# Performance work log

Measured on AMD Instinct MI355X. Metric: run time of the kernel, lower is better.

Reference implementation:

```python
import jax, jax.numpy as jnp
import numpy as np

EPS = 1e-5
SCALE = 30.0

def _ln(x, g, b):
    m = jnp.mean(x, axis=-1, keepdims=True)
    v = jnp.mean((x - m) ** 2, axis=-1, keepdims=True)
    return (x - m) * jax.lax.rsqrt(v + EPS) * g + b

def setup_inputs() -> dict:
    key = jax.random.key(0)
    ks = jax.random.split(key, 12)
    B, L, K, H, NIN = 4, 2048, 48, 128, 512
    s = 0.02
    return {
        "h_V": jax.random.normal(ks[0], (B, L, H), jnp.float32),
        "h_E": jax.random.normal(ks[1], (B, L, K, NIN - H), jnp.float32),
        "mask_V": jnp.ones((B, L), jnp.float32),
        "mask_E": jnp.ones((B, L, K), jnp.float32),
        "w1": jax.random.normal(ks[2], (NIN, H), jnp.float32) * s,
        "b1": jnp.zeros((H,), jnp.float32),
        "w2": jax.random.normal(ks[3], (H, H), jnp.float32) * s,
        "b2": jnp.zeros((H,), jnp.float32),
        "w3": jax.random.normal(ks[4], (H, H), jnp.float32) * s,
        "b3": jnp.zeros((H,), jnp.float32),
        "g1": jnp.ones((H,), jnp.float32),
        "bn1": jnp.zeros((H,), jnp.float32),
        "g2": jnp.ones((H,), jnp.float32),
        "bn2": jnp.zeros((H,), jnp.float32),
        "wf1": jax.random.normal(ks[5], (H, 4 * H), jnp.float32) * s,
        "bf1": jnp.zeros((4 * H,), jnp.float32),
        "wf2": jax.random.normal(ks[6], (4 * H, H), jnp.float32) * s,
        "bf2": jnp.zeros((H,), jnp.float32),
    }

def reference(h_V, h_E, mask_V, mask_E, w1, b1, w2, b2, w3, b3, g1, bn1, g2, bn2, wf1, bf1, wf2, bf2):
    B, L, H = h_V.shape
    K = h_E.shape[-2]
    gelu = lambda x: jax.nn.gelu(x, approximate=False)  # torch nn.GELU default (erf)
    # expand source node over K neighbors and concat: (B,L,K,num_in)
    h_V_exp = jnp.broadcast_to(h_V[:, :, None, :], (B, L, K, H))
    h_EV = jnp.concatenate([h_V_exp, h_E], axis=-1)
    h_msg = gelu(jnp.einsum('blki,ih->blkh', h_EV, w1) + b1)
    h_msg = gelu(jnp.einsum('blkh,hj->blkj', h_msg, w2) + b2)
    h_msg = jnp.einsum('blkh,hj->blkj', h_msg, w3) + b3
    h_msg = mask_E[..., None] * h_msg
    dh = jnp.sum(h_msg, axis=-2) / SCALE  # masked sum-aggregate over K
    h = _ln(h_V + dh, g1, bn1)
    dff = jnp.einsum('blh,hf->blf', h, wf1) + bf1
    dff = jnp.einsum('blf,fh->blh', gelu(dff), wf2) + bf2
    h = _ln(h + dff, g2, bn2)
    return mask_V[..., None] * h
```

## Files before the change

kernel.cpp:

```cpp
#include <hip/hip_runtime.h>
#include <hip/hip_bf16.h>


typedef __bf16 bf16x8 __attribute__((ext_vector_type(8)));
typedef float f32x4 __attribute__((ext_vector_type(4)));

#define HH 128
#define EE 384
#define KK 48

__device__ __forceinline__ float gelu_f(float x) {
  float x2 = x * x;
  float u = x * (-1.5957691216f - 0.0713548163f * x2);
  float e = __expf(u);
  return __fdividef(x, 1.0f + e);
}

__device__ __forceinline__ bf16x8 cvt8(float4 a, float4 b) {
  bf16x8 r;
  r[0] = (__bf16)a.x; r[1] = (__bf16)a.y; r[2] = (__bf16)a.z; r[3] = (__bf16)a.w;
  r[4] = (__bf16)b.x; r[5] = (__bf16)b.y; r[6] = (__bf16)b.z; r[7] = (__bf16)b.w;
  return r;
}

__device__ __forceinline__ f32x4 mfma16(bf16x8 a, bf16x8 b, f32x4 c) {
  return __builtin_amdgcn_mfma_f32_16x16x32_bf16(a, b, c, 0, 0, 0);
}

__global__ void prep_kernel(const float* __restrict__ w1, const float* __restrict__ w2,
                            const float* __restrict__ w3, const float* __restrict__ wf1,
                            const float* __restrict__ wf2, __bf16* __restrict__ out) {
  int idx = blockIdx.x * 256 + threadIdx.x;
  if (idx < 49152) {
    int n = idx / 384, e = idx - n * 384;
    out[idx] = (__bf16)w1[(128 + e) * 128 + n];
  } else if (idx < 65536) {
    int t = idx - 49152; int j = t >> 7, h = t & 127;
    out[idx] = (__bf16)w2[h * 128 + j];
  } else if (idx < 81920) {
    int t = idx - 65536; int j = t >> 7, h = t & 127;
    out[idx] = (__bf16)w3[h * 128 + j];
  } else if (idx < 147456) {
    int t = idx - 81920; int f = t >> 7, h = t & 127;
    out[idx] = (__bf16)wf1[h * 512 + f];
  } else if (idx < 212992) {
    int t = idx - 147456; int h = t >> 9, f = t & 511;
    out[idx] = (__bf16)wf2[f * 128 + h];
  }
}

__global__ __launch_bounds__(128) void v1_kernel(const float* __restrict__ hV,
                                                 const float* __restrict__ w1,
                                                 const float* __restrict__ b1,
                                                 float* __restrict__ V1) {
  __shared__ __align__(16) float sV[16][128];
  const int tid = threadIdx.x;
  const long p0 = (long)blockIdx.x * 16;
  for (int i = 0; i < 16; ++i) sV[i][tid] = hV[(p0 + i) * HH + tid];
  __syncthreads();
  float acc[16];
  float bb = b1[tid];
  #pragma unroll
  for (int p = 0; p < 16; ++p) acc[p] = bb;
  for (int k = 0; k < 128; k += 4) {
    float wa = w1[(k + 0) * HH + tid];
    float wb = w1[(k + 1) * HH + tid];
    float wc = w1[(k + 2) * HH + tid];
    float wd = w1[(k + 3) * HH + tid];
    #pragma unroll
    for (int p = 0; p < 16; ++p) {
      float4 h4 = *(const float4*)&sV[p][k];
      acc[p] = fmaf(h4.x, wa, fmaf(h4.y, wb, fmaf(h4.z, wc, fmaf(h4.w, wd, acc[p]))));
    }
  }
  #pragma unroll
  for (int p = 0; p < 16; ++p) V1[(p0 + p) * HH + tid] = acc[p];
}

__global__ __launch_bounds__(256, 2) void msg_kernel(
    const float* __restrict__ hE, const float* __restrict__ hV,
    const float* __restrict__ maskE,
    const __bf16* __restrict__ w1t, const __bf16* __restrict__ w2t,
    const __bf16* __restrict__ w3t, const float* __restrict__ V1,
    const float* __restrict__ b2, const float* __restrict__ b3,
    const float* __restrict__ g1, const float* __restrict__ bn1,
    float* __restrict__ outH) {
  __shared__ __align__(16) __bf16 sA[192][40];
  __shared__ __align__(16) __bf16 sB[128][40];
  __shared__ __align__(16) __bf16 sH[192][136];
  __shared__ float sDH[4][128];
  __shared__ float sMask[192];

  const int tid = threadIdx.x;
  const int lane = tid & 63;
  const int w = tid >> 6;
  const long pos0 = (long)blockIdx.x * 4;
  const long rowBase = pos0 * KK;
  const int fr = lane & 15;
  const int fg = lane >> 4;

  if (tid < 192) sMask[tid] = maskE[rowBase + tid];

  f32x4 acc[3][8];
  #pragma unroll
  for (int m = 0; m < 3; ++m)
    #pragma unroll
    for (int n = 0; n < 8; ++n) acc[m][n] = (f32x4){0.f, 0.f, 0.f, 0.f};

  const int srow = tid >> 2;
  const int scol = (tid & 3) * 8;

  for (int kc = 0; kc < 12; ++kc) {
    const int k0 = kc * 32;
    #pragma unroll
    for (int pass = 0; pass < 3; ++pass) {
      int row = srow + pass * 64;
      const float* src = hE + (rowBase + row) * EE + k0 + scol;
      float4 v0 = *(const float4*)src;
      float4 v1 = *(const float4*)(src + 4);
      *(bf16x8*)&sA[row][scol] = cvt8(v0, v1);
    }
    {
      int n = tid >> 1, kk = (tid & 1) * 16;
      const __bf16* src = w1t + n * EE + k0 + kk;
      *(bf16x8*)&sB[n][kk] = *(const bf16x8*)src;
      *(bf16x8*)&sB[n][kk + 8] = *(const bf16x8*)(src + 8);
    }
    __syncthreads();
    bf16x8 af[3];
    #pragma unroll
    for (int m = 0; m < 3; ++m) af[m] = *(const bf16x8*)&sA[w * 48 + m * 16 + fr][fg * 8];
    #pragma unroll
    for (int n = 0; n < 8; ++n) {
      bf16x8 bfr = *(const bf16x8*)&sB[n * 16 + fr][fg * 8];
      #pragma unroll
      for (int m = 0; m < 3; ++m) acc[m][n] = mfma16(af[m], bfr, acc[m][n]);
    }
    __syncthreads();
  }
  {
    const float* v1p = V1 + (pos0 + w) * HH;
    #pragma unroll
    for (int n = 0; n < 8; ++n) {
      float v1v = v1p[n * 16 + fr];
      #pragma unroll
      for (int m = 0; m < 3; ++m) {
        #pragma unroll
        for (int j = 0; j < 4; ++j)
          sH[w * 48 + m * 16 + fg * 4 + j][n * 16 + fr] = (__bf16)gelu_f(acc[m][n][j] + v1v);
        acc[m][n] = (f32x4){0.f, 0.f, 0.f, 0.f};
      }
    }
  }
  __syncthreads();

  for (int kc = 0; kc < 4; ++kc) {
    const int k0 = kc * 32;
    {
      int n = tid >> 1, kk = (tid & 1) * 16;
      const __bf16* src = w2t + n * HH + k0 + kk;
      *(bf16x8*)&sB[n][kk] = *(const bf16x8*)src;
      *(bf16x8*)&sB[n][kk + 8] = *(const bf16x8*)(src + 8);
    }
    __syncthreads();
    bf16x8 af[3];
    #pragma unroll
    for (int m = 0; m < 3; ++m) af[m] = *(const bf16x8*)&sH[w * 48 + m * 16 + fr][k0 + fg * 8];
    #pragma unroll
    for (int n = 0; n < 8; ++n) {
      bf16x8 bfr = *(const bf16x8*)&sB[n * 16 + fr][fg * 8];
      #pragma unroll
      for (int m = 0; m < 3; ++m) acc[m][n] = mfma16(af[m], bfr, acc[m][n]);
    }
    __syncthreads();
  }
  {
    #pragma unroll
    for (int n = 0; n < 8; ++n) {
      float b2v = b2[n * 16 + fr];
      #pragma unroll
      for (int m = 0; m < 3; ++m) {
        #pragma unroll
        for (int j = 0; j < 4; ++j)
          sH[w * 48 + m * 16 + fg * 4 + j][n * 16 + fr] = (__bf16)gelu_f(acc[m][n][j] + b2v);
        acc[m][n] = (f32x4){0.f, 0.f, 0.f, 0.f};
      }
    }
  }
  __syncthreads();

  for (int kc = 0; kc < 4; ++kc) {
    const int k0 = kc * 32;
    {
      int n = tid >> 1, kk = (tid & 1) * 16;
      const __bf16* src = w3t + n * HH + k0 + kk;
      *(bf16x8*)&sB[n][kk] = *(const bf16x8*)src;
      *(bf16x8*)&sB[n][kk + 8] = *(const bf16x8*)(src + 8);
    }
    __syncthreads();
    bf16x8 af[3];
    #pragma unroll
    for (int m = 0; m < 3; ++m) af[m] = *(const bf16x8*)&sH[w * 48 + m * 16 + fr][k0 + fg * 8];
    #pragma unroll
    for (int n = 0; n < 8; ++n) {
      bf16x8 bfr = *(const bf16x8*)&sB[n * 16 + fr][fg * 8];
      #pragma unroll
      for (int m = 0; m < 3; ++m) acc[m][n] = mfma16(af[m], bfr, acc[m][n]);
    }
    __syncthreads();
  }

  #pragma unroll
  for (int n = 0; n < 8; ++n) {
    float b3v = b3[n * 16 + fr];
    float s = 0.f;
    #pragma unroll
    for (int m = 0; m < 3; ++m) {
      #pragma unroll
      for (int j = 0; j < 4; ++j)
        s += sMask[w * 48 + m * 16 + fg * 4 + j] * (acc[m][n][j] + b3v);
    }
    s += __shfl_xor(s, 16);
    s += __shfl_xor(s, 32);
    if (lane < 16) sDH[w][n * 16 + lane] = s;
  }
  __syncthreads();

  {
    const long p = pos0 + w;
    float x0 = hV[p * HH + lane] + sDH[w][lane] * (1.f / 30.f);
    float x1 = hV[p * HH + lane + 64] + sDH[w][lane + 64] * (1.f / 30.f);
    float s = x0 + x1;
    #pragma unroll
    for (int off = 32; off >= 1; off >>= 1) s += __shfl_xor(s, off);
    float mean = s * (1.f / 128.f);
    float e0 = x0 - mean, e1 = x1 - mean;
    float q = e0 * e0 + e1 * e1;
    #pragma unroll
    for (int off = 32; off >= 1; off >>= 1) q += __shfl_xor(q, off);
    float rs = rsqrtf(q * (1.f / 128.f) + 1e-5f);
    outH[p * HH + lane] = e0 * rs * g1[lane] + bn1[lane];
    outH[p * HH + lane + 64] = e1 * rs * g1[lane + 64] + bn1[lane + 64];
  }
}

__global__ __launch_bounds__(256, 2) void ffn_kernel(
    const float* __restrict__ xin, const __bf16* __restrict__ wf1t,
    const float* __restrict__ bf1, const __bf16* __restrict__ wf2t,
    const float* __restrict__ bf2, const float* __restrict__ g2,
    const float* __restrict__ bn2, const float* __restrict__ maskV,
    float* __restrict__ out) {
  __shared__ __align__(16) __bf16 sX[32][136];
  __shared__ __align__(16) __bf16 sH1[32][520];
  __shared__ __align__(16) float sOut[32][132];
  const int tid = threadIdx.x, lane = tid & 63, w = tid >> 6;
  const long row0 = (long)blockIdx.x * 32;
  const int fr = lane & 15, fg = lane >> 4;

  {
    int r = tid >> 3, c = (tid & 7) * 16;
    const float* src = xin + (row0 + r) * HH + c;
    float4 v0 = *(const float4*)src, v1 = *(const float4*)(src + 4);
    float4 v2 = *(const float4*)(src + 8), v3 = *(const float4*)(src + 12);
    *(bf16x8*)&sX[r][c] = cvt8(v0, v1);
    *(bf16x8*)&sX[r][c + 8] = cvt8(v2, v3);
  }
  __syncthreads();

  f32x4 a1[2][8];
  #pragma unroll
  for (int m = 0; m < 2; ++m)
    #pragma unroll
    for (int n = 0; n < 8; ++n) a1[m][n] = (f32x4){0.f, 0.f, 0.f, 0.f};
  for (int kc = 0; kc < 4; ++kc) {
    int k0 = kc * 32;
    bf16x8 af0 = *(const bf16x8*)&sX[fr][k0 + fg * 8];
    bf16x8 af1 = *(const bf16x8*)&sX[16 + fr][k0 + fg * 8];
    #pragma unroll
    for (int n = 0; n < 8; ++n) {
      const __bf16* bp = wf1t + (long)(w * 128 + n * 16 + fr) * HH + k0 + fg * 8;
      bf16x8 bfr = *(const bf16x8*)bp;
      a1[0][n] = mfma16(af0, bfr, a1[0][n]);
      a1[1][n] = mfma16(af1, bfr, a1[1][n]);
    }
  }
  #pragma unroll
  for (int n = 0; n < 8; ++n) {
    float bv = bf1[w * 128 + n * 16 + fr];
    #pragma unroll
    for (int m = 0; m < 2; ++m)
      #pragma unroll
      for (int j = 0; j < 4; ++j)
        sH1[m * 16 + fg * 4 + j][w * 128 + n * 16 + fr] = (__bf16)gelu_f(a1[m][n][j] + bv);
  }
  __syncthreads();

  f32x4 a2[2][2];
  #pragma unroll
  for (int m = 0; m < 2; ++m)
    #pragma unroll
    for (int n = 0; n < 2; ++n) a2[m][n] = (f32x4){0.f, 0.f, 0.f, 0.f};
  for (int kc = 0; kc < 16; ++kc) {
    int k0 = kc * 32;
    bf16x8 af0 = *(const bf16x8*)&sH1[fr][k0 + fg * 8];
    bf16x8 af1 = *(const bf16x8*)&sH1[16 + fr][k0 + fg * 8];
    #pragma unroll
    for (int n = 0; n < 2; ++n) {
      const __bf16* bp = wf2t + (long)(w * 32 + n * 16 + fr) * 512 + k0 + fg * 8;
      bf16x8 bfr = *(const bf16x8*)bp;
      a2[0][n] = mfma16(af0, bfr, a2[0][n]);
      a2[1][n] = mfma16(af1, bfr, a2[1][n]);
    }
  }
  #pragma unroll
  for (int n = 0; n < 2; ++n) {
    float bv = bf2[w * 32 + n * 16 + fr];
    #pragma unroll
    for (int m = 0; m < 2; ++m)
      #pragma unroll
      for (int j = 0; j < 4; ++j)
        sOut[m * 16 + fg * 4 + j][w * 32 + n * 16 + fr] = a2[m][n][j] + bv;
  }
  __syncthreads();

  {
    int r = tid >> 3, c0 = (tid & 7) * 16;
    long p = row0 + r;
    const float* xp = xin + p * HH + c0;
    float x[16];
    #pragma unroll
    for (int i = 0; i < 16; ++i) x[i] = xp[i] + sOut[r][c0 + i];
    float s = 0.f;
    #pragma unroll
    for (int i = 0; i < 16; ++i) s += x[i];
    s += __shfl_xor(s, 1); s += __shfl_xor(s, 2); s += __shfl_xor(s, 4);
    float mean = s * (1.f / 128.f);
    float q = 0.f;
    #pragma unroll
    for (int i = 0; i < 16; ++i) { float e = x[i] - mean; q += e * e; }
    q += __shfl_xor(q, 1); q += __shfl_xor(q, 2); q += __shfl_xor(q, 4);
    float rs = rsqrtf(q * (1.f / 128.f) + 1e-5f);
    float mv = maskV[p];
    float* op = out + p * HH + c0;
    #pragma unroll
    for (int i = 0; i < 16; ++i)
      op[i] = ((x[i] - mean) * rs * g2[c0 + i] + bn2[c0 + i]) * mv;
  }
}

extern "C" void kernel_launch(void* const* d_in, const int* in_sizes, int n_in,
                              void* d_out, int out_size, void* d_ws, size_t ws_size,
                              hipStream_t stream) {
  const float* hV    = (const float*)d_in[0];
  const float* hE    = (const float*)d_in[1];
  const float* maskV = (const float*)d_in[2];
  const float* maskE = (const float*)d_in[3];
  const float* w1    = (const float*)d_in[4];
  const float* b1    = (const float*)d_in[5];
  const float* w2    = (const float*)d_in[6];
  const float* b2    = (const float*)d_in[7];
  const float* w3    = (const float*)d_in[8];
  const float* b3    = (const float*)d_in[9];
  const float* g1    = (const float*)d_in[10];
  const float* bn1   = (const float*)d_in[11];
  const float* g2    = (const float*)d_in[12];
  const float* bn2   = (const float*)d_in[13];
  const float* wf1   = (const float*)d_in[14];
  const float* bf1   = (const float*)d_in[15];
  const float* wf2   = (const float*)d_in[16];
  const float* bf2   = (const float*)d_in[17];
  float* out = (float*)d_out;

  __bf16* wsb = (__bf16*)d_ws;
  float* V1   = (float*)((char*)d_ws + 425984);
  float* hbuf = (float*)((char*)d_ws + 4620288);

  prep_kernel<<<832, 256, 0, stream>>>(w1, w2, w3, wf1, wf2, wsb);
  v1_kernel<<<512, 128, 0, stream>>>(hV, w1, b1, V1);
  msg_kernel<<<2048, 256, 0, stream>>>(hE, hV, maskE,
                                       wsb, wsb + 49152, wsb + 65536, V1,
                                       b2, b3, g1, bn1, hbuf);
  ffn_kernel<<<256, 256, 0, stream>>>(hbuf, wsb + 81920, bf1, wsb + 147456, bf2,
                                      g2, bn2, maskV, out);
}
```

Measured before the change: 241.5 us.

## Load MFMA operands straight from global memory and drop LDS staging and barriers

The message kernel no longer stages h_E tiles and weight tiles through shared memory. Each wave now loads its own h_E rows and the weight fragments directly from global memory into registers, converts them to bf16 in registers, and feeds the MFMAs. The edge mask is also kept in registers. Because each wave now touches only its own rows of sH and sDH, every __syncthreads is removed and shared-memory use shrinks. The aim is to cut LDS traffic and barrier stalls on this bandwidth-heavy loop. In exchange, each of the four waves fetches the same weight fragments redundantly through the caches, and the fully unrolled loops raise register pressure under the (256,2) launch bounds, with some risk of spilling.

```diff
diff --git a/kernel.cpp b/kernel.cpp
--- a/kernel.cpp
+++ b/kernel.cpp
@@ -85,11 +85,8 @@
     const float* __restrict__ b2, const float* __restrict__ b3,
     const float* __restrict__ g1, const float* __restrict__ bn1,
     float* __restrict__ outH) {
-  __shared__ __align__(16) __bf16 sA[192][40];
-  __shared__ __align__(16) __bf16 sB[128][40];
   __shared__ __align__(16) __bf16 sH[192][136];
   __shared__ float sDH[4][128];
-  __shared__ float sMask[192];
 
   const int tid = threadIdx.x;
   const int lane = tid & 63;
@@ -99,7 +96,10 @@
   const int fr = lane & 15;
   const int fg = lane >> 4;
 
-  if (tid < 192) sMask[tid] = maskE[rowBase + tid];
+  f32x4 mk[3];
+  #pragma unroll
+  for (int m = 0; m < 3; ++m)
+    mk[m] = *(const f32x4*)&maskE[rowBase + w * 48 + m * 16 + fg * 4];
 
   f32x4 acc[3][8];
   #pragma unroll
@@ -107,36 +107,31 @@
     #pragma unroll
     for (int n = 0; n < 8; ++n) acc[m][n] = (f32x4){0.f, 0.f, 0.f, 0.f};
 
-  const int srow = tid >> 2;
-  const int scol = (tid & 3) * 8;
-
+  const float* aBase[3];
+  #pragma unroll
+  for (int m = 0; m < 3; ++m)
+    aBase[m] = hE + (rowBase + w * 48 + m * 16 + fr) * (long)EE + fg * 8;
+
+  #pragma unroll
   for (int kc = 0; kc < 12; ++kc) {
     const int k0 = kc * 32;
-    #pragma unroll
-    for (int pass = 0; pass < 3; ++pass) {
-      int row = srow + pass * 64;
-      const float* src = hE + (rowBase + row) * EE + k0 + scol;
-      float4 v0 = *(const float4*)src;
-      float4 v1 = *(const float4*)(src + 4);
-      *(bf16x8*)&sA[row][scol] = cvt8(v0, v1);
-    }
-    {
-      int n = tid >> 1, kk = (tid & 1) * 16;
-      const __bf16* src = w1t + n * EE + k0 + kk;
-      *(bf16x8*)&sB[n][kk] = *(const bf16x8*)src;
-      *(bf16x8*)&sB[n][kk + 8] = *(const bf16x8*)(src + 8);
-    }
-    __syncthreads();
+    float4 a0[3], a1[3];
+    #pragma unroll
+    for (int m = 0; m < 3; ++m) {
+      a0[m] = *(const float4*)(aBase[m] + k0);
+      a1[m] = *(const float4*)(aBase[m] + k0 + 4);
+    }
+    bf16x8 bfr[8];
+    #pragma unroll
+    for (int n = 0; n < 8; ++n)
+      bfr[n] = *(const bf16x8*)(w1t + (n * 16 + fr) * EE + k0 + fg * 8);
     bf16x8 af[3];
     #pragma unroll
-    for (int m = 0; m < 3; ++m) af[m] = *(const bf16x8*)&sA[w * 48 + m * 16 + fr][fg * 8];
-    #pragma unroll
-    for (int n = 0; n < 8; ++n) {
-      bf16x8 bfr = *(const bf16x8*)&sB[n * 16 + fr][fg * 8];
-      #pragma unroll
-      for (int m = 0; m < 3; ++m) acc[m][n] = mfma16(af[m], bfr, acc[m][n]);
-    }
-    __syncthreads();
+    for (int m = 0; m < 3; ++m) af[m] = cvt8(a0[m], a1[m]);
+    #pragma unroll
+    for (int n = 0; n < 8; ++n)
+      #pragma unroll
+      for (int m = 0; m < 3; ++m) acc[m][n] = mfma16(af[m], bfr[n], acc[m][n]);
   }
   {
     const float* v1p = V1 + (pos0 + w) * HH;
@@ -152,27 +147,22 @@
       }
     }
   }
-  __syncthreads();
-
+
+  #pragma unroll
   for (int kc = 0; kc < 4; ++kc) {
     const int k0 = kc * 32;
-    {
-      int n = tid >> 1, kk = (tid & 1) * 16;
-      const __bf16* src = w2t + n * HH + k0 + kk;
-      *(bf16x8*)&sB[n][kk] = *(const bf16x8*)src;
-      *(bf16x8*)&sB[n][kk + 8] = *(const bf16x8*)(src + 8);
-    }
-    __syncthreads();
+    bf16x8 bfr[8];
+    #pragma unroll
+    for (int n = 0; n < 8; ++n)
+      bfr[n] = *(const bf16x8*)(w2t + (n * 16 + fr) * HH + k0 + fg * 8);
     bf16x8 af[3];
     #pragma unroll
-    for (int m = 0; m < 3; ++m) af[m] = *(const bf16x8*)&sH[w * 48 + m * 16 + fr][k0 + fg * 8];
-    #pragma unroll
-    for (int n = 0; n < 8; ++n) {
-      bf16x8 bfr = *(const bf16x8*)&sB[n * 16 + fr][fg * 8];
-      #pragma unroll
-      for (int m = 0; m < 3; ++m) acc[m][n] = mfma16(af[m], bfr, acc[m][n]);
-    }
-    __syncthreads();
+    for (int m = 0; m < 3; ++m)
+      af[m] = *(const bf16x8*)&sH[w * 48 + m * 16 + fr][k0 + fg * 8];
+    #pragma unroll
+    for (int n = 0; n < 8; ++n)
+      #pragma unroll
+      for (int m = 0; m < 3; ++m) acc[m][n] = mfma16(af[m], bfr[n], acc[m][n]);
   }
   {
     #pragma unroll
@@ -187,27 +177,22 @@
       }
     }
   }
-  __syncthreads();
-
+
+  #pragma unroll
   for (int kc = 0; kc < 4; ++kc) {
     const int k0 = kc * 32;
-    {
-      int n = tid >> 1, kk = (tid & 1) * 16;
-      const __bf16* src = w3t + n * HH + k0 + kk;
-      *(bf16x8*)&sB[n][kk] = *(const bf16x8*)src;
-      *(bf16x8*)&sB[n][kk + 8] = *(const bf16x8*)(src + 8);
-    }
-    __syncthreads();
+    bf16x8 bfr[8];
+    #pragma unroll
+    for (int n = 0; n < 8; ++n)
+      bfr[n] = *(const bf16x8*)(w3t + (n * 16 + fr) * HH + k0 + fg * 8);
     bf16x8 af[3];
     #pragma unroll
-    for (int m = 0; m < 3; ++m) af[m] = *(const bf16x8*)&sH[w * 48 + m * 16 + fr][k0 + fg * 8];
-    #pragma unroll
-    for (int n = 0; n < 8; ++n) {
-      bf16x8 bfr = *(const bf16x8*)&sB[n * 16 + fr][fg * 8];
-      #pragma unroll
-      for (int m = 0; m < 3; ++m) acc[m][n] = mfma16(af[m], bfr, acc[m][n]);
-    }
-    __syncthreads();
+    for (int m = 0; m < 3; ++m)
+      af[m] = *(const bf16x8*)&sH[w * 48 + m * 16 + fr][k0 + fg * 8];
+    #pragma unroll
+    for (int n = 0; n < 8; ++n)
+      #pragma unroll
+      for (int m = 0; m < 3; ++m) acc[m][n] = mfma16(af[m], bfr[n], acc[m][n]);
   }
 
   #pragma unroll
@@ -218,13 +203,12 @@
     for (int m = 0; m < 3; ++m) {
       #pragma unroll
       for (int j = 0; j < 4; ++j)
-        s += sMask[w * 48 + m * 16 + fg * 4 + j] * (acc[m][n][j] + b3v);
+        s += mk[m][j] * (acc[m][n][j] + b3v);
     }
     s += __shfl_xor(s, 16);
     s += __shfl_xor(s, 32);
     if (lane < 16) sDH[w][n * 16 + lane] = s;
   }
-  __syncthreads();
 
   {
     const long p = pos0 + w;
```

Measured after the change: 340.0 us. 40.8% more time.
